# Kernel optimization log

Measured on AMD Instinct MI355X. Metric: run time of the kernel, lower is better.

Reference implementation:

```python
import jax, jax.numpy as jnp
import numpy as np
import math

B, S, DK, DV = 8, 2048, 128, 128
SQRT_DK = math.sqrt(DK)


def setup_inputs() -> dict:
    key = jax.random.key(0)
    kq, kk, kv = jax.random.split(key, 3)
    Q = jax.random.normal(kq, (B, S, DK), dtype=jnp.float32)
    K = jax.random.normal(kk, (B, S, DK), dtype=jnp.float32)
    V = jax.random.normal(kv, (B, S, DV), dtype=jnp.float32)
    # additive causal mask, broadcast over batch: 0 on/below diag, -1e9 above
    causal = jnp.tril(jnp.ones((S, S), dtype=bool))
    mask = jnp.where(causal, 0.0, -1e9).astype(jnp.float32)[None]  # [1, S, S]
    return {"Q": Q, "K": K, "V": V, "mask": mask}


def reference(Q, K, V, mask):
    # QK = Q @ K^T / sqrt(dk); dropout is identity in eval mode.
    scores = jnp.einsum("bqd,bkd->bqk", Q, K) / SQRT_DK + mask  # [B, S, S]
    # transpose->softmax(dim=1)->transpose == softmax over key axis (last dim)
    A = jax.nn.softmax(scores, axis=-1)
    return jnp.einsum("bqk,bkv->bqv", A, V)  # [B, S, DV]
```

## Files before the change

### kernel.cpp

```cpp
#include <hip/hip_runtime.h>

#define SEQ 2048
#define DHEAD 128
#define NB 8
#define KST 136
#define VST 72
#define PST 72

typedef short short8 __attribute__((ext_vector_type(8)));
typedef float f32x4 __attribute__((ext_vector_type(4)));

__device__ __constant__ unsigned char UNIT[80] = {
    124,125,126,127, 120,121,122, 116,117,118, 112,113,114, 108,109,110,
    104,105,106, 96,97,98, 100,101,102, 92,93,94, 88,89, 84,85, 80,81,
    76,77, 72,73, 68,69, 64,65, 60,61, 56, 52, 48, 44, 40, 36, 32, 28,
    123, 90, 57, 24,
    119, 86, 53, 20,
    115, 82, 49, 16,
    111, 78, 45, 12,
    107, 74, 41,  8,
    103, 70, 37,  4,
     99, 66, 33,  0
};

__device__ __forceinline__ unsigned short f2bf(float x) {
    unsigned int u = __float_as_uint(x);
    u += 0x7fffu + ((u >> 16) & 1u);
    return (unsigned short)(u >> 16);
}

__global__ void prep(const float* __restrict__ K, const float* __restrict__ V,
                     unsigned short* __restrict__ Kb, unsigned short* __restrict__ Vt) {
    if (blockIdx.x < 2048) {
        int i = blockIdx.x * 256 + threadIdx.x;
        float4 v = ((const float4*)K)[i];
        ushort4 o;
        o.x = f2bf(v.x); o.y = f2bf(v.y); o.z = f2bf(v.z); o.w = f2bf(v.w);
        ((ushort4*)Kb)[i] = o;
    } else {
        __shared__ unsigned short t[32][33];
        int bx = blockIdx.x - 2048;
        int b = bx >> 8, xy = bx & 255;
        int s0 = (xy >> 2) << 5;
        int d0 = (xy & 3) << 5;
        int tid = threadIdx.x;
        int sl = tid >> 3, dl = (tid & 7) << 2;
        float4 v = *(const float4*)&V[(b * SEQ + s0 + sl) * DHEAD + d0 + dl];
        t[sl][dl + 0] = f2bf(v.x); t[sl][dl + 1] = f2bf(v.y);
        t[sl][dl + 2] = f2bf(v.z); t[sl][dl + 3] = f2bf(v.w);
        __syncthreads();
        int dr = tid >> 3, sr = (tid & 7) << 2;
        ushort4 o;
        o.x = t[sr + 0][dr]; o.y = t[sr + 1][dr]; o.z = t[sr + 2][dr]; o.w = t[sr + 3][dr];
        *(ushort4*)&Vt[(b * DHEAD + d0 + dr) * SEQ + s0 + sr] = o;
    }
}

__global__ __launch_bounds__(256, 3)
void flash_attn(const float* __restrict__ Q, const unsigned short* __restrict__ Kb,
                const unsigned short* __restrict__ Vt,
                float* __restrict__ Opart, float* __restrict__ lsumP,
                float* __restrict__ out) {
    __shared__ __align__(16) unsigned short Klds[64 * KST];
    __shared__ __align__(16) unsigned short Vlds[128 * VST];
    __shared__ __align__(16) unsigned short Pb[4][16 * PST];

    const int b = blockIdx.x & 7;
    const int e = UNIT[blockIdx.x >> 3];
    const int qt = e >> 2, c = e & 3;
    const int kt0 = c * 8;
    const int kt1 = min(qt + 1, kt0 + 8);

    const int tid = threadIdx.x;
    const int w = tid >> 6, lane = tid & 63;
    const int ln15 = lane & 15, g = lane >> 4;
    const int qrow0 = qt * 64 + w * 16;

    const float scale = 0.08838834764831845f;
    short8 qf[4];
    {
        const float* qp = Q + (b * SEQ + qrow0 + ln15) * DHEAD + g * 8;
#pragma unroll
        for (int cc = 0; cc < 4; ++cc) {
            float4 a = *(const float4*)(qp + cc * 32);
            float4 d = *(const float4*)(qp + cc * 32 + 4);
            short8 f;
            f[0] = f2bf(a.x * scale); f[1] = f2bf(a.y * scale);
            f[2] = f2bf(a.z * scale); f[3] = f2bf(a.w * scale);
            f[4] = f2bf(d.x * scale); f[5] = f2bf(d.y * scale);
            f[6] = f2bf(d.z * scale); f[7] = f2bf(d.w * scale);
            qf[cc] = f;
        }
    }

    f32x4 acc[8];
#pragma unroll
    for (int j = 0; j < 8; ++j) acc[j] = (f32x4){0.f, 0.f, 0.f, 0.f};
    float lsum = 0.f;
    unsigned short* P = &Pb[w][0];

    {
        const int k0 = kt0 << 6;
        short8 pre[8];
#pragma unroll
        for (int j = 0; j < 4; ++j) {
            int ck = tid + j * 256;
            pre[j]     = *(const short8*)(Kb + (b * SEQ + k0 + (ck >> 4)) * DHEAD + (ck & 15) * 8);
            pre[4 + j] = *(const short8*)(Vt + (b * DHEAD + (ck >> 3)) * SEQ + k0 + (ck & 7) * 8);
        }
#pragma unroll
        for (int j = 0; j < 4; ++j) {
            int ck = tid + j * 256;
            *(short8*)&Klds[(ck >> 4) * KST + (ck & 15) * 8] = pre[j];
            *(short8*)&Vlds[(ck >> 3) * VST + (ck & 7) * 8]  = pre[4 + j];
        }
    }
    __syncthreads();

    for (int kt = kt0; kt < kt1; ++kt) {
        const int k0 = kt << 6;
        const bool have_next = (kt + 1 < kt1);
        short8 pre2[8];
        if (have_next) {
            const int kn = (kt + 1) << 6;
#pragma unroll
            for (int j = 0; j < 4; ++j) {
                int ck = tid + j * 256;
                pre2[j]     = *(const short8*)(Kb + (b * SEQ + kn + (ck >> 4)) * DHEAD + (ck & 15) * 8);
                pre2[4 + j] = *(const short8*)(Vt + (b * DHEAD + (ck >> 3)) * SEQ + kn + (ck & 7) * 8);
            }
        }

        if (k0 <= qrow0 + 15) {
            const bool nm = (k0 + 63 > qrow0);
#pragma unroll
            for (int mtp = 0; mtp < 2; ++mtp) {
                short8 kf[8];
#pragma unroll
                for (int cc = 0; cc < 4; ++cc) {
                    kf[cc]     = *(const short8*)&Klds[((2 * mtp) * 16 + ln15) * KST + cc * 32 + g * 8];
                    kf[4 + cc] = *(const short8*)&Klds[((2 * mtp + 1) * 16 + ln15) * KST + cc * 32 + g * 8];
                }
                f32x4 s0 = (f32x4){0.f, 0.f, 0.f, 0.f};
                f32x4 s1 = (f32x4){0.f, 0.f, 0.f, 0.f};
#pragma unroll
                for (int cc = 0; cc < 4; ++cc) {
                    s0 = __builtin_amdgcn_mfma_f32_16x16x32_bf16(kf[cc],     qf[cc], s0, 0, 0, 0);
                    s1 = __builtin_amdgcn_mfma_f32_16x16x32_bf16(kf[4 + cc], qf[cc], s1, 0, 0, 0);
                }
#pragma unroll
                for (int h = 0; h < 2; ++h) {
                    f32x4 s = h ? s1 : s0;
                    const int mt = 2 * mtp + h;
                    float p[4];
#pragma unroll
                    for (int r = 0; r < 4; ++r) {
                        p[r] = __expf(s[r]);
                        if (nm) {
                            int colg = k0 + mt * 16 + g * 4 + r;
                            int rowg = qrow0 + ln15;
                            p[r] = (colg <= rowg) ? p[r] : 0.f;
                        }
                    }
                    lsum += (p[0] + p[1]) + (p[2] + p[3]);
                    uint2 dd;
                    dd.x = __builtin_amdgcn_perm(__float_as_uint(p[1]), __float_as_uint(p[0]), 0x07060302u);
                    dd.y = __builtin_amdgcn_perm(__float_as_uint(p[3]), __float_as_uint(p[2]), 0x07060302u);
                    *(uint2*)&P[ln15 * PST + mt * 16 + g * 4] = dd;
                }
            }
#pragma unroll
            for (int c2 = 0; c2 < 2; ++c2) {
                short8 vf[8];
#pragma unroll
                for (int nt2 = 0; nt2 < 8; ++nt2)
                    vf[nt2] = *(const short8*)&Vlds[(nt2 * 16 + ln15) * VST + c2 * 32 + g * 8];
                short8 pf = *(const short8*)&P[ln15 * PST + c2 * 32 + g * 8];
#pragma unroll
                for (int nt2 = 0; nt2 < 8; ++nt2)
                    acc[nt2] = __builtin_amdgcn_mfma_f32_16x16x32_bf16(pf, vf[nt2], acc[nt2], 0, 0, 0);
            }
        }

        if (have_next) {
            __syncthreads();
#pragma unroll
            for (int j = 0; j < 4; ++j) {
                int ck = tid + j * 256;
                *(short8*)&Klds[(ck >> 4) * KST + (ck & 15) * 8] = pre2[j];
                *(short8*)&Vlds[(ck >> 3) * VST + (ck & 7) * 8]  = pre2[4 + j];
            }
            __syncthreads();
        }
    }

    {
        float v = lsum;
        v += __shfl_xor(v, 16);
        v += __shfl_xor(v, 32);
        lsum = v;
    }

    if (qt < 8) {
        float inv[4];
#pragma unroll
        for (int r = 0; r < 4; ++r) inv[r] = 1.0f / __shfl(lsum, g * 4 + r);
#pragma unroll
        for (int nt2 = 0; nt2 < 8; ++nt2) {
#pragma unroll
            for (int r = 0; r < 4; ++r) {
                int rowg = qrow0 + g * 4 + r;
                out[(b * SEQ + rowg) * DHEAD + nt2 * 16 + ln15] = acc[nt2][r] * inv[r];
            }
        }
    } else {
        if (lane < 16)
            lsumP[(c * NB + b) * 1536 + qrow0 + lane - 512] = lsum;
#pragma unroll
        for (int nt2 = 0; nt2 < 8; ++nt2) {
#pragma unroll
            for (int r = 0; r < 4; ++r) {
                int r2 = qrow0 + g * 4 + r - 512;
                Opart[((c * NB + b) * 1536 + r2) * DHEAD + nt2 * 16 + ln15] = acc[nt2][r];
            }
        }
    }
}

__global__ void finalize(const float* __restrict__ Opart, const float* __restrict__ lsumP,
                         float* __restrict__ out) {
    int b = blockIdx.y;
    int gx = blockIdx.x * 256 + threadIdx.x;
    int d4 = gx & 31;
    int r2 = gx >> 5;
    int row = 512 + r2;
    int nch = (row >> 9) + 1;
    float4 o = {0.f, 0.f, 0.f, 0.f};
    float l = 0.f;
    for (int cc = 0; cc < nch; ++cc) {
        float4 p = ((const float4*)Opart)[((cc * NB + b) * 1536 + r2) * 32 + d4];
        o.x += p.x; o.y += p.y; o.z += p.z; o.w += p.w;
        l += lsumP[(cc * NB + b) * 1536 + r2];
    }
    float inv = 1.0f / l;
    float4 r;
    r.x = o.x * inv; r.y = o.y * inv; r.z = o.z * inv; r.w = o.w * inv;
    ((float4*)out)[(b * SEQ + row) * 32 + d4] = r;
}

extern "C" void kernel_launch(void* const* d_in, const int* in_sizes, int n_in,
                              void* d_out, int out_size, void* d_ws, size_t ws_size,
                              hipStream_t stream) {
    const float* Q = (const float*)d_in[0];
    const float* K = (const float*)d_in[1];
    const float* V = (const float*)d_in[2];
    float* out = (float*)d_out;

    const int NE = NB * SEQ * DHEAD;
    unsigned short* Kb = (unsigned short*)d_ws;
    unsigned short* Vt = Kb + NE;
    float* Opart = (float*)(Vt + NE);
    float* lsumP = Opart + 4 * NB * 1536 * DHEAD;

    prep<<<4096, 256, 0, stream>>>(K, V, Kb, Vt);
    flash_attn<<<640, 256, 0, stream>>>(Q, Kb, Vt, Opart, lsumP, out);
    finalize<<<dim3(192, NB), 256, 0, stream>>>(Opart, lsumP, out);
}
```

Before: 110.4 us.

## Store split-K partial outputs in bf16 and batch all four score tiles

```diff
diff --git a/kernel.cpp b/kernel.cpp
--- a/kernel.cpp
+++ b/kernel.cpp
@@ -27,6 +27,10 @@
     unsigned int u = __float_as_uint(x);
     u += 0x7fffu + ((u >> 16) & 1u);
     return (unsigned short)(u >> 16);
+}
+
+__device__ __forceinline__ float bf2f(unsigned short h) {
+    return __uint_as_float(((unsigned int)h) << 16);
 }
 
 __global__ void prep(const float* __restrict__ K, const float* __restrict__ V,
@@ -59,7 +63,7 @@
 __global__ __launch_bounds__(256, 3)
 void flash_attn(const float* __restrict__ Q, const unsigned short* __restrict__ Kb,
                 const unsigned short* __restrict__ Vt,
-                float* __restrict__ Opart, float* __restrict__ lsumP,
+                unsigned short* __restrict__ Opart, float* __restrict__ lsumP,
                 float* __restrict__ out) {
     __shared__ __align__(16) unsigned short Klds[64 * KST];
     __shared__ __align__(16) unsigned short Vlds[128 * VST];
@@ -133,41 +137,37 @@
 
         if (k0 <= qrow0 + 15) {
             const bool nm = (k0 + 63 > qrow0);
-#pragma unroll
-            for (int mtp = 0; mtp < 2; ++mtp) {
-                short8 kf[8];
-#pragma unroll
-                for (int cc = 0; cc < 4; ++cc) {
-                    kf[cc]     = *(const short8*)&Klds[((2 * mtp) * 16 + ln15) * KST + cc * 32 + g * 8];
-                    kf[4 + cc] = *(const short8*)&Klds[((2 * mtp + 1) * 16 + ln15) * KST + cc * 32 + g * 8];
+            short8 kf[16];
+#pragma unroll
+            for (int mt = 0; mt < 4; ++mt)
+#pragma unroll
+                for (int cc = 0; cc < 4; ++cc)
+                    kf[mt * 4 + cc] = *(const short8*)&Klds[(mt * 16 + ln15) * KST + cc * 32 + g * 8];
+            f32x4 s[4];
+#pragma unroll
+            for (int mt = 0; mt < 4; ++mt) s[mt] = (f32x4){0.f, 0.f, 0.f, 0.f};
+#pragma unroll
+            for (int cc = 0; cc < 4; ++cc)
+#pragma unroll
+                for (int mt = 0; mt < 4; ++mt)
+                    s[mt] = __builtin_amdgcn_mfma_f32_16x16x32_bf16(kf[mt * 4 + cc], qf[cc], s[mt], 0, 0, 0);
+#pragma unroll
+            for (int mt = 0; mt < 4; ++mt) {
+                float p[4];
+#pragma unroll
+                for (int r = 0; r < 4; ++r) {
+                    p[r] = __expf(s[mt][r]);
+                    if (nm) {
+                        int colg = k0 + mt * 16 + g * 4 + r;
+                        int rowg = qrow0 + ln15;
+                        p[r] = (colg <= rowg) ? p[r] : 0.f;
+                    }
                 }
-                f32x4 s0 = (f32x4){0.f, 0.f, 0.f, 0.f};
-                f32x4 s1 = (f32x4){0.f, 0.f, 0.f, 0.f};
-#pragma unroll
-                for (int cc = 0; cc < 4; ++cc) {
-                    s0 = __builtin_amdgcn_mfma_f32_16x16x32_bf16(kf[cc],     qf[cc], s0, 0, 0, 0);
-                    s1 = __builtin_amdgcn_mfma_f32_16x16x32_bf16(kf[4 + cc], qf[cc], s1, 0, 0, 0);
-                }
-#pragma unroll
-                for (int h = 0; h < 2; ++h) {
-                    f32x4 s = h ? s1 : s0;
-                    const int mt = 2 * mtp + h;
-                    float p[4];
-#pragma unroll
-                    for (int r = 0; r < 4; ++r) {
-                        p[r] = __expf(s[r]);
-                        if (nm) {
-                            int colg = k0 + mt * 16 + g * 4 + r;
-                            int rowg = qrow0 + ln15;
-                            p[r] = (colg <= rowg) ? p[r] : 0.f;
-                        }
-                    }
-                    lsum += (p[0] + p[1]) + (p[2] + p[3]);
-                    uint2 dd;
-                    dd.x = __builtin_amdgcn_perm(__float_as_uint(p[1]), __float_as_uint(p[0]), 0x07060302u);
-                    dd.y = __builtin_amdgcn_perm(__float_as_uint(p[3]), __float_as_uint(p[2]), 0x07060302u);
-                    *(uint2*)&P[ln15 * PST + mt * 16 + g * 4] = dd;
-                }
+                lsum += (p[0] + p[1]) + (p[2] + p[3]);
+                uint2 dd;
+                dd.x = __builtin_amdgcn_perm(__float_as_uint(p[1]), __float_as_uint(p[0]), 0x07060302u);
+                dd.y = __builtin_amdgcn_perm(__float_as_uint(p[3]), __float_as_uint(p[2]), 0x07060302u);
+                *(uint2*)&P[ln15 * PST + mt * 16 + g * 4] = dd;
             }
 #pragma unroll
             for (int c2 = 0; c2 < 2; ++c2) {
@@ -221,14 +221,14 @@
 #pragma unroll
             for (int r = 0; r < 4; ++r) {
                 int r2 = qrow0 + g * 4 + r - 512;
-                Opart[((c * NB + b) * 1536 + r2) * DHEAD + nt2 * 16 + ln15] = acc[nt2][r];
-            }
-        }
-    }
-}
-
-__global__ void finalize(const float* __restrict__ Opart, const float* __restrict__ lsumP,
-                         float* __restrict__ out) {
+                Opart[((c * NB + b) * 1536 + r2) * DHEAD + nt2 * 16 + ln15] = f2bf(acc[nt2][r]);
+            }
+        }
+    }
+}
+
+__global__ void finalize(const unsigned short* __restrict__ Opart,
+                         const float* __restrict__ lsumP, float* __restrict__ out) {
     int b = blockIdx.y;
     int gx = blockIdx.x * 256 + threadIdx.x;
     int d4 = gx & 31;
@@ -238,8 +238,8 @@
     float4 o = {0.f, 0.f, 0.f, 0.f};
     float l = 0.f;
     for (int cc = 0; cc < nch; ++cc) {
-        float4 p = ((const float4*)Opart)[((cc * NB + b) * 1536 + r2) * 32 + d4];
-        o.x += p.x; o.y += p.y; o.z += p.z; o.w += p.w;
+        ushort4 ph = ((const ushort4*)Opart)[((cc * NB + b) * 1536 + r2) * 32 + d4];
+        o.x += bf2f(ph.x); o.y += bf2f(ph.y); o.z += bf2f(ph.z); o.w += bf2f(ph.w);
         l += lsumP[(cc * NB + b) * 1536 + r2];
     }
     float inv = 1.0f / l;
@@ -259,8 +259,8 @@
     const int NE = NB * SEQ * DHEAD;
     unsigned short* Kb = (unsigned short*)d_ws;
     unsigned short* Vt = Kb + NE;
-    float* Opart = (float*)(Vt + NE);
-    float* lsumP = Opart + 4 * NB * 1536 * DHEAD;
+    unsigned short* Opart = Vt + NE;
+    float* lsumP = (float*)(Opart + 4 * NB * 1536 * DHEAD);
 
     prep<<<4096, 256, 0, stream>>>(K, V, Kb, Vt);
     flash_attn<<<640, 256, 0, stream>>>(Q, Kb, Vt, Opart, lsumP, out);
```

New measurement: 115.0 us. 4.2% more time.
